# Optimization experiments

Measured on AMD Instinct MI355X. Metric: run time of the kernel, lower is better.

## Reference

```python
import jax, jax.numpy as jnp
import numpy as np

D_MODEL = 1024
D_STATE = 16
LN_EPS = 1e-5


def setup_inputs() -> dict:
    key = jax.random.key(0)
    ks = jax.random.split(key, 10)
    B, L, D, N = 4, 1024, D_MODEL, D_STATE
    s = lambda fan_in: 1.0 / np.sqrt(fan_in)
    x_in = jax.random.normal(ks[0], (B, L, D), dtype=jnp.float32)
    W_in = jax.random.uniform(ks[1], (D, 2 * D), jnp.float32, -s(D), s(D))
    W_x = jax.random.uniform(ks[2], (D, D + 2 * N), jnp.float32, -s(D), s(D))
    W_dt = jax.random.uniform(ks[3], (D, D), jnp.float32, -s(D), s(D))
    b_dt = jax.random.uniform(ks[4], (D,), jnp.float32, -4.0, -1.0)
    A_log = jnp.tile(jnp.log(jnp.arange(1, N + 1, dtype=jnp.float32))[None, :], (D, 1))
    D_param = jnp.ones((D,), dtype=jnp.float32)
    W_out = jax.random.uniform(ks[5], (D, D), jnp.float32, -s(D), s(D))
    ln_g = jnp.ones((D,), dtype=jnp.float32)
    ln_b = jnp.zeros((D,), dtype=jnp.float32)
    return {"x_in": x_in, "W_in": W_in, "W_x": W_x, "W_dt": W_dt, "b_dt": b_dt,
            "A_log": A_log, "D_param": D_param, "W_out": W_out, "ln_g": ln_g, "ln_b": ln_b}


def reference(x_in, W_in, W_x, W_dt, b_dt, A_log, D_param, W_out, ln_g, ln_b):
    B, L, D = x_in.shape
    N = A_log.shape[1]
    xz = x_in @ W_in                       # [B,L,2D]
    x, z = xz[..., :D], xz[..., D:]
    proj = x @ W_x                         # [B,L,D+2N]
    delta_raw = proj[..., :D]
    B_ssm = proj[..., D:D + N]
    C_ssm = proj[..., D + N:]
    delta = jax.nn.softplus(delta_raw @ W_dt + b_dt)   # [B,L,D]
    A = -jnp.exp(A_log)                    # [D,N]
    dA = jnp.exp(jnp.einsum('bld,dn->bldn', delta, A))      # [B,L,D,N]
    dBx = jnp.einsum('bld,bln->bldn', delta * x, B_ssm)      # dB * x, fused

    def step(h, inp):
        dA_t, dBx_t, C_t = inp             # [B,D,N],[B,D,N],[B,N]
        h = dA_t * h + dBx_t
        y_t = jnp.einsum('bdn,bn->bd', h, C_t)
        return h, y_t

    h0 = jnp.zeros((B, D, N), dtype=x.dtype)
    xs = (jnp.moveaxis(dA, 1, 0), jnp.moveaxis(dBx, 1, 0), jnp.moveaxis(C_ssm, 1, 0))
    _, ys = jax.lax.scan(step, h0, xs)     # ys: [L,B,D]
    y = jnp.moveaxis(ys, 0, 1) + x * D_param
    y = (y * jax.nn.silu(z)) @ W_out
    res = y + x_in
    mu = jnp.mean(res, axis=-1, keepdims=True)
    var = jnp.var(res, axis=-1, keepdims=True)
    return (res - mu) * jax.lax.rsqrt(var + LN_EPS) * ln_g + ln_b
```

## Files before the change

### kernel.cpp

```cpp
#include <hip/hip_runtime.h>

#define D_MODEL 1024
#define D_STATE 16
#define M_ROWS  4096
#define SEQ_L   1024
#define NSEG    32
#define LSEG    32

typedef __bf16 bf16x8 __attribute__((ext_vector_type(8)));
typedef float  f32x4  __attribute__((ext_vector_type(4)));

__device__ __forceinline__ unsigned short f2bf(float f) {
  unsigned int u = __builtin_bit_cast(unsigned int, f);
  u += 0x7fffu + ((u >> 16) & 1u);
  return (unsigned short)(u >> 16);
}
__device__ __forceinline__ float bf2f(unsigned short b) {
  unsigned int u = ((unsigned int)b) << 16;
  return __builtin_bit_cast(float, u);
}
__device__ __forceinline__ float load_elem(const void* p, size_t i, int isbf) {
  if (isbf) return bf2f(((const unsigned short*)p)[i]);
  return ((const float*)p)[i];
}

__device__ __forceinline__ void gload16(const void* g, void* l) {
  typedef const __attribute__((address_space(1))) unsigned int GU;
  typedef __attribute__((address_space(3))) unsigned int LU;
  __builtin_amdgcn_global_load_lds((GU*)(unsigned long long)g,
                                   (LU*)(unsigned int)(unsigned long long)l,
                                   16, 0, 0);
}

__global__ void detect_kernel(const unsigned short* __restrict__ x, int* __restrict__ flag) {
  __shared__ int cnt;
  if (threadIdx.x == 0) cnt = 0;
  __syncthreads();
  unsigned int v = x[2 * threadIdx.x];
  unsigned int e = (v >> 7) & 0xFFu;
  int ok = (e >= 100u && e <= 135u) ? 1 : 0;
  atomicAdd(&cnt, ok);
  __syncthreads();
  if (threadIdx.x == 0) *flag = (cnt >= 128) ? 1 : 0;
}

__global__ void convert_x_kernel(const void* __restrict__ src, float* __restrict__ dstf,
                                 unsigned short* __restrict__ dstb,
                                 const int* __restrict__ flag) {
  int c = blockIdx.x * blockDim.x + threadIdx.x;
  int isbf = *flag;
  float o[8];
  if (isbf) {
    uint4 v = ((const uint4*)src)[c];
    o[0] = bf2f((unsigned short)(v.x & 0xffffu)); o[1] = bf2f((unsigned short)(v.x >> 16));
    o[2] = bf2f((unsigned short)(v.y & 0xffffu)); o[3] = bf2f((unsigned short)(v.y >> 16));
    o[4] = bf2f((unsigned short)(v.z & 0xffffu)); o[5] = bf2f((unsigned short)(v.z >> 16));
    o[6] = bf2f((unsigned short)(v.w & 0xffffu)); o[7] = bf2f((unsigned short)(v.w >> 16));
    ((uint4*)dstb)[c] = v;
  } else {
    float4 a = ((const float4*)src)[2 * c];
    float4 b = ((const float4*)src)[2 * c + 1];
    o[0]=a.x; o[1]=a.y; o[2]=a.z; o[3]=a.w; o[4]=b.x; o[5]=b.y; o[6]=b.z; o[7]=b.w;
    uint4 p;
    p.x = (unsigned int)f2bf(o[0]) | ((unsigned int)f2bf(o[1]) << 16);
    p.y = (unsigned int)f2bf(o[2]) | ((unsigned int)f2bf(o[3]) << 16);
    p.z = (unsigned int)f2bf(o[4]) | ((unsigned int)f2bf(o[5]) << 16);
    p.w = (unsigned int)f2bf(o[6]) | ((unsigned int)f2bf(o[7]) << 16);
    ((uint4*)dstb)[c] = p;
  }
  float4* d = (float4*)dstf;
  d[2*c]   = make_float4(o[0], o[1], o[2], o[3]);
  d[2*c+1] = make_float4(o[4], o[5], o[6], o[7]);
}

__global__ void convert_smalls_kernel(const void* b_dt, const void* A_log, const void* Dp,
                                      const void* ln_g, const void* ln_b,
                                      float* o_bdt, float* o_a2, float* o_dp,
                                      float* o_lng, float* o_lnb,
                                      const int* __restrict__ flag) {
  int g = blockIdx.x * blockDim.x + threadIdx.x;
  int isbf = *flag;
  if (g < 1024)              o_bdt[g]          = load_elem(b_dt, g, isbf);
  else if (g < 17408) {
    float v = load_elem(A_log, g - 1024, isbf);
    o_a2[g - 1024] = -expf(v) * 1.4426950408889634f;
  }
  else if (g < 18432)        o_dp[g - 17408]   = load_elem(Dp, g - 17408, isbf);
  else if (g < 19456)        o_lng[g - 18432]  = load_elem(ln_g, g - 18432, isbf);
  else                       o_lnb[g - 19456]  = load_elem(ln_b, g - 19456, isbf);
}

__global__ void transpose_w_kernel(const void* __restrict__ src, unsigned short* __restrict__ dst,
                                   int ncols, const int* __restrict__ flag) {
  __shared__ float tile[32][33];
  int tx = threadIdx.x, ty = threadIdx.y;
  int n0 = blockIdx.x * 32, k0 = blockIdx.y * 32;
  int isbf = *flag;
  #pragma unroll
  for (int r = 0; r < 4; ++r) {
    int k = k0 + ty + r * 8;
    int n = n0 + tx;
    float v = (n < ncols) ? load_elem(src, (size_t)k * ncols + n, isbf) : 0.f;
    tile[ty + r * 8][tx] = v;
  }
  __syncthreads();
  #pragma unroll
  for (int r = 0; r < 4; ++r) {
    int n = n0 + ty + r * 8;
    int k = k0 + tx;
    dst[(size_t)n * 1024 + k] = f2bf(tile[tx][ty + r * 8]);
  }
}

template<int MODE>
__global__ __launch_bounds__(256, 3) void gemm_bf(
    const unsigned short* __restrict__ A, const unsigned short* __restrict__ Bt,
    void* __restrict__ o0, void* __restrict__ o1, float* __restrict__ o2f,
    const float* __restrict__ aux) {
  constexpr int NITER = D_MODEL / 32;
  __shared__ __align__(16) unsigned short a_lds[3][128 * 32];
  __shared__ __align__(16) unsigned short b_lds[3][128 * 32];
  const int tid = threadIdx.x;
  const int m0 = blockIdx.x * 128, n0 = blockIdx.y * 128;
  const int wave = tid >> 6, lane = tid & 63;
  const int wr = (wave >> 1) * 64, wc = (wave & 1) * 64;
  const int lrow = lane & 15, quad = lane >> 4;

  const int srow = wave * 32 + (lane >> 2);
  const int sc = (lane & 3) ^ ((lane >> 3) & 3);
  const unsigned short* gA  = A  + (size_t)(m0 + srow) * 1024 + sc * 8;
  const unsigned short* gA2 = gA + 16 * 1024;
  const unsigned short* gB  = Bt + (size_t)(n0 + srow) * 1024 + sc * 8;
  const unsigned short* gB2 = gB + 16 * 1024;
  const int soff = wave * 32 * 32;

  const int q2 = quad ^ ((lrow >> 1) & 3);

  f32x4 acc[4][4];
  #pragma unroll
  for (int i = 0; i < 4; ++i)
    #pragma unroll
    for (int jj = 0; jj < 4; ++jj)
      #pragma unroll
      for (int r = 0; r < 4; ++r) acc[i][jj][r] = 0.f;

  auto issue = [&](int k) {
    unsigned short* ab = &a_lds[k % 3][soff];
    unsigned short* bb = &b_lds[k % 3][soff];
    gload16(gA  + k * 32, ab);
    gload16(gA2 + k * 32, ab + 16 * 32);
    gload16(gB  + k * 32, bb);
    gload16(gB2 + k * 32, bb + 16 * 32);
  };
  auto compute = [&](int k) {
    const unsigned short* ard = &a_lds[k % 3][(wr + lrow) * 32 + q2 * 8];
    const unsigned short* brd = &b_lds[k % 3][(wc + lrow) * 32 + q2 * 8];
    bf16x8 af[4], bfr[4];
    #pragma unroll
    for (int i = 0; i < 4; ++i) {
      af[i]  = *(const bf16x8*)(ard + i * 16 * 32);
      bfr[i] = *(const bf16x8*)(brd + i * 16 * 32);
    }
    #pragma unroll
    for (int i = 0; i < 4; ++i)
      #pragma unroll
      for (int jj = 0; jj < 4; ++jj)
        acc[i][jj] = __builtin_amdgcn_mfma_f32_16x16x32_bf16(af[i], bfr[jj], acc[i][jj], 0, 0, 0);
  };

  issue(0);
  issue(1);
  #pragma unroll
  for (int k = 0; k < NITER - 1; ++k) {
    asm volatile("s_waitcnt vmcnt(4)" ::: "memory");
    __builtin_amdgcn_s_barrier();
    if (k + 2 < NITER) issue(k + 2);
    compute(k);
  }
  asm volatile("s_waitcnt vmcnt(0)" ::: "memory");
  __builtin_amdgcn_s_barrier();
  compute(NITER - 1);

  #pragma unroll
  for (int i = 0; i < 4; ++i) {
    #pragma unroll
    for (int jj = 0; jj < 4; ++jj) {
      #pragma unroll
      for (int r = 0; r < 4; ++r) {
        int m = m0 + wr + i * 16 + quad * 4 + r;
        int n = n0 + wc + jj * 16 + lrow;
        float v = acc[i][jj][r];
        if (MODE == 1) {
          if (n < D_MODEL) {
            ((unsigned short*)o0)[(size_t)m * D_MODEL + n] = f2bf(v);
          } else {
            float sig = 1.f / (1.f + expf(-v));
            ((unsigned short*)o1)[(size_t)m * D_MODEL + (n - D_MODEL)] = f2bf(v * sig);
          }
        } else if (MODE == 2) {
          if (n < D_MODEL)                  ((unsigned short*)o0)[(size_t)m * D_MODEL + n] = f2bf(v);
          else if (n < D_MODEL + D_STATE)   ((float*)o1)[(size_t)m * D_STATE + (n - D_MODEL)] = v;
          else if (n < D_MODEL + 2*D_STATE) o2f[(size_t)m * D_STATE + (n - D_MODEL - D_STATE)] = v;
        } else if (MODE == 3) {
          float t = v + aux[n];
          float sp = (t > 20.f) ? t : log1pf(expf(t));
          ((unsigned short*)o0)[(size_t)m * D_MODEL + n] = f2bf(sp);
        } else {
          ((float*)o0)[(size_t)m * D_MODEL + n] = v + aux[(size_t)m * D_MODEL + n];
        }
      }
    }
  }
}

template<int PHASE>
__global__ __launch_bounds__(256) void scan_phase(
    const unsigned short* __restrict__ dl_bf, const unsigned short* __restrict__ x_bf,
    const unsigned short* __restrict__ z_bf, const float* __restrict__ Bs,
    const float* __restrict__ Cs, const float* __restrict__ A2g,
    const float* __restrict__ Dpar, const float* __restrict__ hinit,
    float* __restrict__ Hout, float* __restrict__ sdout,
    unsigned short* __restrict__ g) {
  __shared__ float4 bsh[LSEG][4];
  __shared__ float4 csh[LSEG][4];
  const int tid = threadIdx.x;
  const int bid = blockIdx.x;
  const int seg = bid >> 4;
  const int b = (bid >> 2) & 3;
  const int dc = bid & 3;
  const int d = dc * 256 + tid;
  const int t0 = seg * LSEG;
  const int bd = b * D_MODEL + d;

  if (tid < 128) {
    int r = tid >> 2, q = tid & 3;
    size_t src = ((size_t)b * SEQ_L + t0 + r) * 4 + q;
    bsh[r][q] = ((const float4*)Bs)[src];
    if (PHASE == 1) csh[r][q] = ((const float4*)Cs)[src];
  }

  float A2r[16];
  {
    const float4* a4 = (const float4*)(A2g + (size_t)d * 16);
    #pragma unroll
    for (int q = 0; q < 4; ++q) {
      float4 v = a4[q];
      A2r[4*q] = v.x; A2r[4*q+1] = v.y; A2r[4*q+2] = v.z; A2r[4*q+3] = v.w;
    }
  }
  float h[16];
  if (PHASE == 1) {
    const float4* h4 = (const float4*)(hinit + (((size_t)seg * 4096) + bd) * 16);
    #pragma unroll
    for (int q = 0; q < 4; ++q) {
      float4 v = h4[q];
      h[4*q] = v.x; h[4*q+1] = v.y; h[4*q+2] = v.z; h[4*q+3] = v.w;
    }
  } else {
    #pragma unroll
    for (int n = 0; n < 16; ++n) h[n] = 0.f;
  }
  const float Dpd = (PHASE == 1) ? Dpar[d] : 0.f;
  float sd = 0.f;
  const size_t base = ((size_t)b * SEQ_L + t0) * D_MODEL + d;
  __syncthreads();

  unsigned short dreg[2][8], xreg[2][8], zreg[2][8];
  #pragma unroll
  for (int t = 0; t < 8; ++t) {
    size_t o = base + (size_t)t * D_MODEL;
    dreg[0][t] = dl_bf[o]; xreg[0][t] = x_bf[o];
    if (PHASE == 1) zreg[0][t] = z_bf[o];
  }
  #pragma unroll
  for (int c = 0; c < LSEG / 8; ++c) {
    const int cur = c & 1, nxt = cur ^ 1;
    if (c < LSEG / 8 - 1) {
      #pragma unroll
      for (int t = 0; t < 8; ++t) {
        size_t o = base + (size_t)((c + 1) * 8 + t) * D_MODEL;
        dreg[nxt][t] = dl_bf[o]; xreg[nxt][t] = x_bf[o];
        if (PHASE == 1) zreg[nxt][t] = z_bf[o];
      }
    }
    #pragma unroll
    for (int t = 0; t < 8; ++t) {
      const int tt = c * 8 + t;
      float dl = bf2f(dreg[cur][t]);
      float xx = bf2f(xreg[cur][t]);
      float dx = dl * xx;
      sd += dl;
      float4 b0 = bsh[tt][0], b1 = bsh[tt][1], b2 = bsh[tt][2], b3 = bsh[tt][3];
      float bb[16] = {b0.x,b0.y,b0.z,b0.w, b1.x,b1.y,b1.z,b1.w,
                      b2.x,b2.y,b2.z,b2.w, b3.x,b3.y,b3.z,b3.w};
      if (PHASE == 0) {
        #pragma unroll
        for (int n = 0; n < 16; ++n) {
          float dA = exp2f(dl * A2r[n]);
          h[n] = fmaf(dA, h[n], dx * bb[n]);
        }
      } else {
        float4 c0 = csh[tt][0], c1 = csh[tt][1], c2 = csh[tt][2], c3 = csh[tt][3];
        float cc[16] = {c0.x,c0.y,c0.z,c0.w, c1.x,c1.y,c1.z,c1.w,
                        c2.x,c2.y,c2.z,c2.w, c3.x,c3.y,c3.z,c3.w};
        float y = 0.f;
        #pragma unroll
        for (int n = 0; n < 16; ++n) {
          float dA = exp2f(dl * A2r[n]);
          h[n] = fmaf(dA, h[n], dx * bb[n]);
          y = fmaf(h[n], cc[n], y);
        }
        float zz = bf2f(zreg[cur][t]);
        g[base + (size_t)tt * D_MODEL] = f2bf(fmaf(xx, Dpd, y) * zz);
      }
    }
  }
  if (PHASE == 0) {
    float4* ho = (float4*)(Hout + (((size_t)seg * 4096) + bd) * 16);
    #pragma unroll
    for (int q = 0; q < 4; ++q)
      ho[q] = make_float4(h[4*q], h[4*q+1], h[4*q+2], h[4*q+3]);
    sdout[(size_t)seg * 4096 + bd] = sd;
  }
}

__global__ __launch_bounds__(256) void scan_phaseB(
    const float* __restrict__ H, const float* __restrict__ sdelta,
    const float* __restrict__ A2g, float* __restrict__ hinit) {
  int gidx = blockIdx.x * 256 + threadIdx.x;
  int bd = gidx >> 4, n = gidx & 15;
  float A2 = A2g[(size_t)(bd & (D_MODEL - 1)) * 16 + n];
  float hp = 0.f;
  #pragma unroll
  for (int s = 0; s < NSEG; ++s) {
    size_t idx = ((size_t)s * 4096 + bd) * 16 + n;
    hinit[idx] = hp;
    float P = exp2f(A2 * sdelta[(size_t)s * 4096 + bd]);
    hp = fmaf(P, hp, H[idx]);
  }
}

__global__ __launch_bounds__(256) void ln_kernel(const float* __restrict__ res,
    const float* __restrict__ lng, const float* __restrict__ lnb,
    void* __restrict__ out, const int* __restrict__ flag) {
  int row = blockIdx.x, tid = threadIdx.x;
  const float4* r4 = (const float4*)(res + (size_t)row * D_MODEL);
  float4 v = r4[tid];
  float s = v.x + v.y + v.z + v.w;
  float q = v.x * v.x + v.y * v.y + v.z * v.z + v.w * v.w;
  #pragma unroll
  for (int m = 1; m < 64; m <<= 1) { s += __shfl_xor(s, m); q += __shfl_xor(q, m); }
  __shared__ float ss[4], qs[4];
  int w = tid >> 6;
  if ((tid & 63) == 0) { ss[w] = s; qs[w] = q; }
  __syncthreads();
  s = ss[0] + ss[1] + ss[2] + ss[3];
  q = qs[0] + qs[1] + qs[2] + qs[3];
  float mu = s * (1.f / D_MODEL);
  float var = q * (1.f / D_MODEL) - mu * mu;
  float rstd = rsqrtf(var + 1e-5f);
  float4 gg = ((const float4*)lng)[tid];
  float4 bb = ((const float4*)lnb)[tid];
  float o0 = (v.x - mu) * rstd * gg.x + bb.x;
  float o1 = (v.y - mu) * rstd * gg.y + bb.y;
  float o2 = (v.z - mu) * rstd * gg.z + bb.z;
  float o3 = (v.w - mu) * rstd * gg.w + bb.w;
  if (*flag) {
    ushort4 pv;
    pv.x = f2bf(o0); pv.y = f2bf(o1); pv.z = f2bf(o2); pv.w = f2bf(o3);
    ((ushort4*)out)[(size_t)row * 256 + tid] = pv;
  } else {
    ((float4*)out)[(size_t)row * 256 + tid] = make_float4(o0, o1, o2, o3);
  }
}

extern "C" void kernel_launch(void* const* d_in, const int* in_sizes, int n_in,
                              void* d_out, int out_size, void* d_ws, size_t ws_size,
                              hipStream_t stream) {
  (void)in_sizes; (void)n_in; (void)out_size; (void)ws_size;
  const void* x_in  = d_in[0];
  const void* W_in  = d_in[1];
  const void* W_x   = d_in[2];
  const void* W_dt  = d_in[3];
  const void* b_dt  = d_in[4];
  const void* A_log = d_in[5];
  const void* D_par = d_in[6];
  const void* W_out = d_in[7];
  const void* ln_g  = d_in[8];
  const void* ln_b  = d_in[9];

  char* ws = (char*)d_ws;
  size_t off = 0;
  auto alloc = [&](size_t bytes) -> void* {
    void* p = ws + off;
    off += (bytes + 255) & ~(size_t)255;
    return p;
  };
  int* flag              = (int*)alloc(16);
  float* x_in_f          = (float*)alloc((size_t)M_ROWS * D_MODEL * 4);
  unsigned short* x_in_b = (unsigned short*)alloc((size_t)M_ROWS * D_MODEL * 2);
  float* bdt_f           = (float*)alloc(1024 * 4);
  float* a2_f            = (float*)alloc(16384 * 4);
  float* dp_f            = (float*)alloc(1024 * 4);
  float* lng_f           = (float*)alloc(1024 * 4);
  float* lnb_f           = (float*)alloc(1024 * 4);
  unsigned short* wt_in  = (unsigned short*)alloc((size_t)2048 * 1024 * 2);
  unsigned short* wt_x   = (unsigned short*)alloc((size_t)1152 * 1024 * 2);
  unsigned short* wt_dt  = (unsigned short*)alloc((size_t)1024 * 1024 * 2);
  unsigned short* wt_out = (unsigned short*)alloc((size_t)1024 * 1024 * 2);
  unsigned short* x_bf   = (unsigned short*)alloc((size_t)M_ROWS * D_MODEL * 2);
  unsigned short* s_bf   = (unsigned short*)alloc((size_t)M_ROWS * D_MODEL * 2);
  unsigned short* draw_bf= (unsigned short*)alloc((size_t)M_ROWS * D_MODEL * 2);
  unsigned short* delta_bf=(unsigned short*)alloc((size_t)M_ROWS * D_MODEL * 2);
  float* bssm_f          = (float*)alloc((size_t)M_ROWS * D_STATE * 4);
  float* cssm_f          = (float*)alloc((size_t)M_ROWS * D_STATE * 4);
  float* H_f             = (float*)alloc((size_t)NSEG * 4096 * 16 * 4);
  float* hinit_f         = (float*)alloc((size_t)NSEG * 4096 * 16 * 4);
  float* sdelta_f        = (float*)alloc((size_t)NSEG * 4096 * 4);
  unsigned short* g_bf = draw_bf;
  float* res_f = (float*)x_bf;

  detect_kernel<<<1, 256, 0, stream>>>((const unsigned short*)x_in, flag);
  convert_x_kernel<<<2048, 256, 0, stream>>>(x_in, x_in_f, x_in_b, flag);
  convert_smalls_kernel<<<80, 256, 0, stream>>>(b_dt, A_log, D_par, ln_g, ln_b,
                                                bdt_f, a2_f, dp_f, lng_f, lnb_f, flag);
  dim3 tb(32, 8);
  transpose_w_kernel<<<dim3(64, 32), tb, 0, stream>>>(W_in,  wt_in,  2048, flag);
  transpose_w_kernel<<<dim3(36, 32), tb, 0, stream>>>(W_x,   wt_x,   1056, flag);
  transpose_w_kernel<<<dim3(32, 32), tb, 0, stream>>>(W_dt,  wt_dt,  1024, flag);
  transpose_w_kernel<<<dim3(32, 32), tb, 0, stream>>>(W_out, wt_out, 1024, flag);

  gemm_bf<1><<<dim3(32, 16), 256, 0, stream>>>(x_in_b, wt_in, x_bf, s_bf, nullptr, nullptr);
  gemm_bf<2><<<dim3(32, 9),  256, 0, stream>>>(x_bf, wt_x, draw_bf, bssm_f, cssm_f, nullptr);
  gemm_bf<3><<<dim3(32, 8),  256, 0, stream>>>(draw_bf, wt_dt, delta_bf, nullptr, nullptr, bdt_f);

  scan_phase<0><<<512, 256, 0, stream>>>(delta_bf, x_bf, nullptr, bssm_f, nullptr,
                                         a2_f, nullptr, nullptr, H_f, sdelta_f, nullptr);
  scan_phaseB<<<256, 256, 0, stream>>>(H_f, sdelta_f, a2_f, hinit_f);
  scan_phase<1><<<512, 256, 0, stream>>>(delta_bf, x_bf, s_bf, bssm_f, cssm_f,
                                         a2_f, dp_f, hinit_f, nullptr, nullptr, g_bf);

  gemm_bf<4><<<dim3(32, 8),  256, 0, stream>>>(g_bf, wt_out, res_f, nullptr, nullptr, x_in_f);
  ln_kernel<<<4096, 256, 0, stream>>>(res_f, lng_f, lnb_f, d_out, flag);
}
```

Baseline: 289.1 us.

## Shrink GEMM tiles, double scan segments, merge transposes, drop fp32 x copy

GEMM tiles go from 128x128 to 64x128, which doubles the block count and raises the launch bound to 4 blocks per CU for better occupancy. The selective scan now uses 64 segments of 16 steps instead of 32 of 32, giving more parallel blocks in exchange for a longer sequential segment-combine pass (whose unroll was removed). The four weight transposes are merged into one launch. The fp32 copy of x_in is no longer materialized; the residual add reads the original input directly, which saves a large write and read.

```diff
diff --git a/kernel.cpp b/kernel.cpp
--- a/kernel.cpp
+++ b/kernel.cpp
@@ -4,8 +4,8 @@
 #define D_STATE 16
 #define M_ROWS  4096
 #define SEQ_L   1024
-#define NSEG    32
-#define LSEG    32
+#define NSEG    64
+#define LSEG    16
 
 typedef __bf16 bf16x8 __attribute__((ext_vector_type(8)));
 typedef float  f32x4  __attribute__((ext_vector_type(4)));
@@ -44,33 +44,23 @@
   if (threadIdx.x == 0) *flag = (cnt >= 128) ? 1 : 0;
 }
 
-__global__ void convert_x_kernel(const void* __restrict__ src, float* __restrict__ dstf,
+__global__ void convert_x_kernel(const void* __restrict__ src,
                                  unsigned short* __restrict__ dstb,
                                  const int* __restrict__ flag) {
   int c = blockIdx.x * blockDim.x + threadIdx.x;
   int isbf = *flag;
-  float o[8];
   if (isbf) {
-    uint4 v = ((const uint4*)src)[c];
-    o[0] = bf2f((unsigned short)(v.x & 0xffffu)); o[1] = bf2f((unsigned short)(v.x >> 16));
-    o[2] = bf2f((unsigned short)(v.y & 0xffffu)); o[3] = bf2f((unsigned short)(v.y >> 16));
-    o[4] = bf2f((unsigned short)(v.z & 0xffffu)); o[5] = bf2f((unsigned short)(v.z >> 16));
-    o[6] = bf2f((unsigned short)(v.w & 0xffffu)); o[7] = bf2f((unsigned short)(v.w >> 16));
-    ((uint4*)dstb)[c] = v;
+    ((uint4*)dstb)[c] = ((const uint4*)src)[c];
   } else {
     float4 a = ((const float4*)src)[2 * c];
     float4 b = ((const float4*)src)[2 * c + 1];
-    o[0]=a.x; o[1]=a.y; o[2]=a.z; o[3]=a.w; o[4]=b.x; o[5]=b.y; o[6]=b.z; o[7]=b.w;
     uint4 p;
-    p.x = (unsigned int)f2bf(o[0]) | ((unsigned int)f2bf(o[1]) << 16);
-    p.y = (unsigned int)f2bf(o[2]) | ((unsigned int)f2bf(o[3]) << 16);
-    p.z = (unsigned int)f2bf(o[4]) | ((unsigned int)f2bf(o[5]) << 16);
-    p.w = (unsigned int)f2bf(o[6]) | ((unsigned int)f2bf(o[7]) << 16);
+    p.x = (unsigned int)f2bf(a.x) | ((unsigned int)f2bf(a.y) << 16);
+    p.y = (unsigned int)f2bf(a.z) | ((unsigned int)f2bf(a.w) << 16);
+    p.z = (unsigned int)f2bf(b.x) | ((unsigned int)f2bf(b.y) << 16);
+    p.w = (unsigned int)f2bf(b.z) | ((unsigned int)f2bf(b.w) << 16);
     ((uint4*)dstb)[c] = p;
   }
-  float4* d = (float4*)dstf;
-  d[2*c]   = make_float4(o[0], o[1], o[2], o[3]);
-  d[2*c+1] = make_float4(o[4], o[5], o[6], o[7]);
 }
 
 __global__ void convert_smalls_kernel(const void* b_dt, const void* A_log, const void* Dp,
@@ -90,9 +80,20 @@
   else                       o_lnb[g - 19456]  = load_elem(ln_b, g - 19456, isbf);
 }
 
-__global__ void transpose_w_kernel(const void* __restrict__ src, unsigned short* __restrict__ dst,
-                                   int ncols, const int* __restrict__ flag) {
+__global__ void transpose_all_kernel(const void* __restrict__ s0, const void* __restrict__ s1,
+                                     const void* __restrict__ s2, const void* __restrict__ s3,
+                                     unsigned short* __restrict__ d0, unsigned short* __restrict__ d1,
+                                     unsigned short* __restrict__ d2, unsigned short* __restrict__ d3,
+                                     const int* __restrict__ flag) {
   __shared__ float tile[32][33];
+  const void* src; unsigned short* dst; int ncols, nx;
+  switch (blockIdx.z) {
+    case 0:  src = s0; dst = d0; ncols = 2048; nx = 64; break;
+    case 1:  src = s1; dst = d1; ncols = 1056; nx = 33; break;
+    case 2:  src = s2; dst = d2; ncols = 1024; nx = 32; break;
+    default: src = s3; dst = d3; ncols = 1024; nx = 32; break;
+  }
+  if ((int)blockIdx.x >= nx) return;
   int tx = threadIdx.x, ty = threadIdx.y;
   int n0 = blockIdx.x * 32, k0 = blockIdx.y * 32;
   int isbf = *flag;
@@ -113,76 +114,73 @@
 }
 
 template<int MODE>
-__global__ __launch_bounds__(256, 3) void gemm_bf(
-    const unsigned short* __restrict__ A, const unsigned short* __restrict__ Bt,
-    void* __restrict__ o0, void* __restrict__ o1, float* __restrict__ o2f,
-    const float* __restrict__ aux) {
-  constexpr int NITER = D_MODEL / 32;
-  __shared__ __align__(16) unsigned short a_lds[3][128 * 32];
+__global__ __launch_bounds__(256, 4) void gemm_bf(
+    const unsigned short* __restrict__ A, const unsigned short* __restrict__ Bt, int ldb,
+    void* __restrict__ o0, void* __restrict__ o1, void* __restrict__ o2,
+    float* __restrict__ o3, float* __restrict__ o4,
+    const float* __restrict__ aux, const void* __restrict__ auxv,
+    const int* __restrict__ flag) {
+  __shared__ __align__(16) unsigned short a_lds[3][64 * 32];
   __shared__ __align__(16) unsigned short b_lds[3][128 * 32];
   const int tid = threadIdx.x;
-  const int m0 = blockIdx.x * 128, n0 = blockIdx.y * 128;
+  const int m0 = blockIdx.x * 64, n0 = blockIdx.y * 128;
   const int wave = tid >> 6, lane = tid & 63;
-  const int wr = (wave >> 1) * 64, wc = (wave & 1) * 64;
+  const int wr = (wave >> 1) * 32, wc = (wave & 1) * 64;
   const int lrow = lane & 15, quad = lane >> 4;
 
-  const int srow = wave * 32 + (lane >> 2);
   const int sc = (lane & 3) ^ ((lane >> 3) & 3);
-  const unsigned short* gA  = A  + (size_t)(m0 + srow) * 1024 + sc * 8;
-  const unsigned short* gA2 = gA + 16 * 1024;
-  const unsigned short* gB  = Bt + (size_t)(n0 + srow) * 1024 + sc * 8;
-  const unsigned short* gB2 = gB + 16 * 1024;
-  const int soff = wave * 32 * 32;
-
+  const unsigned short* gA  = A  + (size_t)(m0 + wave * 16 + (lane >> 2)) * 1024 + sc * 8;
+  const unsigned short* gB  = Bt + (size_t)(n0 + wave * 32 + (lane >> 2)) * ldb + sc * 8;
+  const unsigned short* gB2 = gB + (size_t)16 * ldb;
   const int q2 = quad ^ ((lrow >> 1) & 3);
 
-  f32x4 acc[4][4];
-  #pragma unroll
-  for (int i = 0; i < 4; ++i)
-    #pragma unroll
-    for (int jj = 0; jj < 4; ++jj)
+  f32x4 acc[2][4];
+  #pragma unroll
+  for (int i = 0; i < 2; ++i)
+    #pragma unroll
+    for (int j = 0; j < 4; ++j)
       #pragma unroll
-      for (int r = 0; r < 4; ++r) acc[i][jj][r] = 0.f;
+      for (int r = 0; r < 4; ++r) acc[i][j][r] = 0.f;
 
   auto issue = [&](int k) {
-    unsigned short* ab = &a_lds[k % 3][soff];
-    unsigned short* bb = &b_lds[k % 3][soff];
-    gload16(gA  + k * 32, ab);
-    gload16(gA2 + k * 32, ab + 16 * 32);
-    gload16(gB  + k * 32, bb);
+    unsigned short* ab = a_lds[k % 3] + wave * 16 * 32;
+    unsigned short* bb = b_lds[k % 3] + wave * 32 * 32;
+    gload16(gA + k * 32, ab);
+    gload16(gB + k * 32, bb);
     gload16(gB2 + k * 32, bb + 16 * 32);
   };
   auto compute = [&](int k) {
-    const unsigned short* ard = &a_lds[k % 3][(wr + lrow) * 32 + q2 * 8];
-    const unsigned short* brd = &b_lds[k % 3][(wc + lrow) * 32 + q2 * 8];
-    bf16x8 af[4], bfr[4];
-    #pragma unroll
-    for (int i = 0; i < 4; ++i) {
-      af[i]  = *(const bf16x8*)(ard + i * 16 * 32);
-      bfr[i] = *(const bf16x8*)(brd + i * 16 * 32);
-    }
-    #pragma unroll
-    for (int i = 0; i < 4; ++i)
+    const unsigned short* ard = a_lds[k % 3] + (wr + lrow) * 32 + q2 * 8;
+    const unsigned short* brd = b_lds[k % 3] + (wc + lrow) * 32 + q2 * 8;
+    bf16x8 af[2], bfr[4];
+    #pragma unroll
+    for (int i = 0; i < 2; ++i) af[i] = *(const bf16x8*)(ard + i * 16 * 32);
+    #pragma unroll
+    for (int j = 0; j < 4; ++j) bfr[j] = *(const bf16x8*)(brd + j * 16 * 32);
+    #pragma unroll
+    for (int i = 0; i < 2; ++i)
       #pragma unroll
-      for (int jj = 0; jj < 4; ++jj)
-        acc[i][jj] = __builtin_amdgcn_mfma_f32_16x16x32_bf16(af[i], bfr[jj], acc[i][jj], 0, 0, 0);
+      for (int j = 0; j < 4; ++j)
+        acc[i][j] = __builtin_amdgcn_mfma_f32_16x16x32_bf16(af[i], bfr[j], acc[i][j], 0, 0, 0);
   };
 
   issue(0);
   issue(1);
   #pragma unroll
-  for (int k = 0; k < NITER - 1; ++k) {
-    asm volatile("s_waitcnt vmcnt(4)" ::: "memory");
+  for (int k = 0; k < 31; ++k) {
+    asm volatile("s_waitcnt vmcnt(3)" ::: "memory");
     __builtin_amdgcn_s_barrier();
-    if (k + 2 < NITER) issue(k + 2);
+    if (k + 2 < 32) issue(k + 2);
     compute(k);
   }
   asm volatile("s_waitcnt vmcnt(0)" ::: "memory");
   __builtin_amdgcn_s_barrier();
-  compute(NITER - 1);
-
-  #pragma unroll
-  for (int i = 0; i < 4; ++i) {
+  compute(31);
+
+  const int isbf = (MODE == 4) ? *flag : 0;
+
+  #pragma unroll
+  for (int i = 0; i < 2; ++i) {
     #pragma unroll
     for (int jj = 0; jj < 4; ++jj) {
       #pragma unroll
@@ -191,22 +189,23 @@
         int n = n0 + wc + jj * 16 + lrow;
         float v = acc[i][jj][r];
         if (MODE == 1) {
-          if (n < D_MODEL) {
-            ((unsigned short*)o0)[(size_t)m * D_MODEL + n] = f2bf(v);
+          if (n < 1024) {
+            ((unsigned short*)o0)[(size_t)m * 1024 + n] = f2bf(v);
           } else {
             float sig = 1.f / (1.f + expf(-v));
-            ((unsigned short*)o1)[(size_t)m * D_MODEL + (n - D_MODEL)] = f2bf(v * sig);
+            ((unsigned short*)o1)[(size_t)m * 1024 + (n - 1024)] = f2bf(v * sig);
           }
         } else if (MODE == 2) {
-          if (n < D_MODEL)                  ((unsigned short*)o0)[(size_t)m * D_MODEL + n] = f2bf(v);
-          else if (n < D_MODEL + D_STATE)   ((float*)o1)[(size_t)m * D_STATE + (n - D_MODEL)] = v;
-          else if (n < D_MODEL + 2*D_STATE) o2f[(size_t)m * D_STATE + (n - D_MODEL - D_STATE)] = v;
+          if (n < 1024)       ((unsigned short*)o0)[(size_t)m * 1024 + n] = f2bf(v);
+          else if (n < 1040)  o3[(size_t)m * D_STATE + (n - 1024)] = v;
+          else if (n < 1056)  o4[(size_t)m * D_STATE + (n - 1040)] = v;
         } else if (MODE == 3) {
           float t = v + aux[n];
           float sp = (t > 20.f) ? t : log1pf(expf(t));
-          ((unsigned short*)o0)[(size_t)m * D_MODEL + n] = f2bf(sp);
+          ((unsigned short*)o0)[(size_t)m * 1024 + n] = f2bf(sp);
         } else {
-          ((float*)o0)[(size_t)m * D_MODEL + n] = v + aux[(size_t)m * D_MODEL + n];
+          ((float*)o0)[(size_t)m * 1024 + n] =
+              v + load_elem(auxv, (size_t)m * 1024 + n, isbf);
         }
       }
     }
@@ -232,7 +231,7 @@
   const int t0 = seg * LSEG;
   const int bd = b * D_MODEL + d;
 
-  if (tid < 128) {
+  if (tid < LSEG * 4) {
     int r = tid >> 2, q = tid & 3;
     size_t src = ((size_t)b * SEQ_L + t0 + r) * 4 + q;
     bsh[r][q] = ((const float4*)Bs)[src];
@@ -331,7 +330,6 @@
   int bd = gidx >> 4, n = gidx & 15;
   float A2 = A2g[(size_t)(bd & (D_MODEL - 1)) * 16 + n];
   float hp = 0.f;
-  #pragma unroll
   for (int s = 0; s < NSEG; ++s) {
     size_t idx = ((size_t)s * 4096 + bd) * 16 + n;
     hinit[idx] = hp;
@@ -396,50 +394,51 @@
     off += (bytes + 255) & ~(size_t)255;
     return p;
   };
-  int* flag              = (int*)alloc(16);
-  float* x_in_f          = (float*)alloc((size_t)M_ROWS * D_MODEL * 4);
-  unsigned short* x_in_b = (unsigned short*)alloc((size_t)M_ROWS * D_MODEL * 2);
-  float* bdt_f           = (float*)alloc(1024 * 4);
-  float* a2_f            = (float*)alloc(16384 * 4);
-  float* dp_f            = (float*)alloc(1024 * 4);
-  float* lng_f           = (float*)alloc(1024 * 4);
-  float* lnb_f           = (float*)alloc(1024 * 4);
-  unsigned short* wt_in  = (unsigned short*)alloc((size_t)2048 * 1024 * 2);
-  unsigned short* wt_x   = (unsigned short*)alloc((size_t)1152 * 1024 * 2);
-  unsigned short* wt_dt  = (unsigned short*)alloc((size_t)1024 * 1024 * 2);
-  unsigned short* wt_out = (unsigned short*)alloc((size_t)1024 * 1024 * 2);
-  unsigned short* x_bf   = (unsigned short*)alloc((size_t)M_ROWS * D_MODEL * 2);
-  unsigned short* s_bf   = (unsigned short*)alloc((size_t)M_ROWS * D_MODEL * 2);
-  unsigned short* draw_bf= (unsigned short*)alloc((size_t)M_ROWS * D_MODEL * 2);
-  unsigned short* delta_bf=(unsigned short*)alloc((size_t)M_ROWS * D_MODEL * 2);
-  float* bssm_f          = (float*)alloc((size_t)M_ROWS * D_STATE * 4);
-  float* cssm_f          = (float*)alloc((size_t)M_ROWS * D_STATE * 4);
-  float* H_f             = (float*)alloc((size_t)NSEG * 4096 * 16 * 4);
-  float* hinit_f         = (float*)alloc((size_t)NSEG * 4096 * 16 * 4);
-  float* sdelta_f        = (float*)alloc((size_t)NSEG * 4096 * 4);
+  int* flag               = (int*)alloc(16);
+  unsigned short* x_in_b  = (unsigned short*)alloc((size_t)M_ROWS * D_MODEL * 2);
+  float* bdt_f            = (float*)alloc(1024 * 4);
+  float* a2_f             = (float*)alloc(16384 * 4);
+  float* dp_f             = (float*)alloc(1024 * 4);
+  float* lng_f            = (float*)alloc(1024 * 4);
+  float* lnb_f            = (float*)alloc(1024 * 4);
+  unsigned short* wt_in   = (unsigned short*)alloc((size_t)2048 * 1024 * 2);
+  unsigned short* wt_x    = (unsigned short*)alloc((size_t)1152 * 1024 * 2);
+  unsigned short* wt_dt   = (unsigned short*)alloc((size_t)1024 * 1024 * 2);
+  unsigned short* wt_out  = (unsigned short*)alloc((size_t)1024 * 1024 * 2);
+  unsigned short* x_bf    = (unsigned short*)alloc((size_t)M_ROWS * D_MODEL * 2);
+  unsigned short* s_bf    = (unsigned short*)alloc((size_t)M_ROWS * D_MODEL * 2);
+  unsigned short* draw_bf = (unsigned short*)alloc((size_t)M_ROWS * D_MODEL * 2);
+  unsigned short* delta_bf= (unsigned short*)alloc((size_t)M_ROWS * D_MODEL * 2);
+  float* bssm_f           = (float*)alloc((size_t)M_ROWS * D_STATE * 4);
+  float* cssm_f           = (float*)alloc((size_t)M_ROWS * D_STATE * 4);
+  float* H_f              = (float*)alloc((size_t)NSEG * 4096 * 16 * 4);
+  float* hinit_f          = (float*)alloc((size_t)NSEG * 4096 * 16 * 4);
+  float* sdelta_f         = (float*)alloc((size_t)NSEG * 4096 * 4);
   unsigned short* g_bf = draw_bf;
   float* res_f = (float*)x_bf;
 
   detect_kernel<<<1, 256, 0, stream>>>((const unsigned short*)x_in, flag);
-  convert_x_kernel<<<2048, 256, 0, stream>>>(x_in, x_in_f, x_in_b, flag);
+  convert_x_kernel<<<2048, 256, 0, stream>>>(x_in, x_in_b, flag);
   convert_smalls_kernel<<<80, 256, 0, stream>>>(b_dt, A_log, D_par, ln_g, ln_b,
                                                 bdt_f, a2_f, dp_f, lng_f, lnb_f, flag);
   dim3 tb(32, 8);
-  transpose_w_kernel<<<dim3(64, 32), tb, 0, stream>>>(W_in,  wt_in,  2048, flag);
-  transpose_w_kernel<<<dim3(36, 32), tb, 0, stream>>>(W_x,   wt_x,   1056, flag);
-  transpose_w_kernel<<<dim3(32, 32), tb, 0, stream>>>(W_dt,  wt_dt,  1024, flag);
-  transpose_w_kernel<<<dim3(32, 32), tb, 0, stream>>>(W_out, wt_out, 1024, flag);
-
-  gemm_bf<1><<<dim3(32, 16), 256, 0, stream>>>(x_in_b, wt_in, x_bf, s_bf, nullptr, nullptr);
-  gemm_bf<2><<<dim3(32, 9),  256, 0, stream>>>(x_bf, wt_x, draw_bf, bssm_f, cssm_f, nullptr);
-  gemm_bf<3><<<dim3(32, 8),  256, 0, stream>>>(draw_bf, wt_dt, delta_bf, nullptr, nullptr, bdt_f);
-
-  scan_phase<0><<<512, 256, 0, stream>>>(delta_bf, x_bf, nullptr, bssm_f, nullptr,
-                                         a2_f, nullptr, nullptr, H_f, sdelta_f, nullptr);
+  transpose_all_kernel<<<dim3(64, 32, 4), tb, 0, stream>>>(
+      W_in, W_x, W_dt, W_out, wt_in, wt_x, wt_dt, wt_out, flag);
+
+  gemm_bf<1><<<dim3(64, 16), 256, 0, stream>>>(x_in_b, wt_in, 1024,
+      x_bf, s_bf, nullptr, nullptr, nullptr, nullptr, nullptr, flag);
+  gemm_bf<2><<<dim3(64, 9), 256, 0, stream>>>(x_bf, wt_x, 1024,
+      draw_bf, nullptr, nullptr, bssm_f, cssm_f, nullptr, nullptr, flag);
+  gemm_bf<3><<<dim3(64, 8), 256, 0, stream>>>(draw_bf, wt_dt, 1024,
+      delta_bf, nullptr, nullptr, nullptr, nullptr, bdt_f, nullptr, flag);
+
+  scan_phase<0><<<1024, 256, 0, stream>>>(delta_bf, x_bf, nullptr, bssm_f, nullptr,
+                                          a2_f, nullptr, nullptr, H_f, sdelta_f, nullptr);
   scan_phaseB<<<256, 256, 0, stream>>>(H_f, sdelta_f, a2_f, hinit_f);
-  scan_phase<1><<<512, 256, 0, stream>>>(delta_bf, x_bf, s_bf, bssm_f, cssm_f,
-                                         a2_f, dp_f, hinit_f, nullptr, nullptr, g_bf);
-
-  gemm_bf<4><<<dim3(32, 8),  256, 0, stream>>>(g_bf, wt_out, res_f, nullptr, nullptr, x_in_f);
+  scan_phase<1><<<1024, 256, 0, stream>>>(delta_bf, x_bf, s_bf, bssm_f, cssm_f,
+                                          a2_f, dp_f, hinit_f, nullptr, nullptr, g_bf);
+
+  gemm_bf<4><<<dim3(64, 8), 256, 0, stream>>>(g_bf, wt_out, 1024,
+      res_f, nullptr, nullptr, nullptr, nullptr, nullptr, x_in, flag);
   ln_kernel<<<4096, 256, 0, stream>>>(res_f, lng_f, lnb_f, d_out, flag);
 }
```

After: 279.6 us. -3.3%, faster.
